# Performance work log

Measured on AMD Instinct MI355X. Metric: run time of the kernel, lower is better.

Reference implementation:

```python
import jax, jax.numpy as jnp
import numpy as np

N_NODES = 100000
N_EDGES = 1600000
IN_C, HID_C, OUT_C = 128, 128, 64


def gcn_conv(x, W, b, src, dst, n_nodes):
    """PyG-style GCNConv: h = x @ W; add self-loops; symmetric deg^-1/2 norm;
    scatter-add aggregation; + bias. Self-loop contribution added analytically
    (norm for self-loop edge i->i is deg_i^-1) instead of materializing edges."""
    h = x @ W  # [N, C_out]
    # degree over dst including self-loops (edge weights are all ones)
    deg = jax.ops.segment_sum(jnp.ones((src.shape[0],), h.dtype), dst,
                              num_segments=n_nodes) + 1.0
    dinv = jax.lax.rsqrt(deg)  # deg >= 1 always
    norm = dinv[src] * dinv[dst]  # [E]
    agg = jax.ops.segment_sum(h[src] * norm[:, None], dst, num_segments=n_nodes)
    agg = agg + h * (dinv * dinv)[:, None]  # self-loop term
    return agg + b


def setup_inputs() -> dict:
    key = jax.random.key(0)
    k0, k1, k2, k3, k4, k5 = jax.random.split(key, 6)
    x = jax.random.normal(k0, (N_NODES, IN_C), dtype=jnp.float32)
    edge_index = jax.random.randint(k1, (2, N_EDGES), 0, N_NODES, dtype=jnp.int64)
    s1 = 1.0 / np.sqrt(IN_C)
    s2 = 1.0 / np.sqrt(HID_C)
    W1 = jax.random.uniform(k2, (IN_C, HID_C), jnp.float32, -s1, s1)
    b1 = jax.random.uniform(k3, (HID_C,), jnp.float32, -s1, s1)
    W2 = jax.random.uniform(k4, (HID_C, OUT_C), jnp.float32, -s2, s2)
    b2 = jax.random.uniform(k5, (OUT_C,), jnp.float32, -s2, s2)
    return {"x": x, "W1": W1, "b1": b1, "W2": W2, "b2": b2,
            "edge_index": edge_index}


def reference(x, W1, b1, W2, b2, edge_index):
    src, dst = edge_index[0], edge_index[1]
    h = gcn_conv(x, W1, b1, src, dst, N_NODES)
    h = jax.nn.relu(h)
    out = gcn_conv(h, W2, b2, src, dst, N_NODES)
    return out
```

## Files before the change

kernel.cpp:

```cpp
#include <hip/hip_runtime.h>


static constexpr int BSHIFT = 7;
static constexpr int BWIDTH = 1 << BSHIFT;
static constexpr int MAXBUCK = 2048;
static constexpr int NPART = 256;

static constexpr size_t OFF_FLAG = 0;
static constexpr size_t OFF_DEG  = 256;
static constexpr size_t OFF_ROW  = 458752;
static constexpr size_t OFF_BSUM = 917504;
static constexpr size_t OFF_CCNT = 925696;
static constexpr size_t OFF_COFF = 937984;
static constexpr size_t OFF_DINV = 962560;
static constexpr size_t OFF_CSR  = 1376256;
static constexpr size_t OFF_HS1  = 8388608;
static constexpr size_t OFF_OUT1 = 35651584;
static constexpr size_t OFF_HS2  = 62914560;
static constexpr size_t OFF_H2   = 75714560;

__device__ __forceinline__ unsigned short f2bf(float f) {
    unsigned u = __float_as_uint(f);
    u += 0x7fffu + ((u >> 16) & 1u);
    return (unsigned short)(u >> 16);
}

typedef __attribute__((ext_vector_type(8))) short bf16x8;
typedef __attribute__((ext_vector_type(4))) float f32x4;

__global__ void detect_kernel(const unsigned* __restrict__ w,
                              unsigned* __restrict__ flag) {
    int i = blockIdx.x * blockDim.x + threadIdx.x;
    if (w[2 * i + 1] != 0u) atomicOr(flag, 1u);
}

__device__ __forceinline__ int edge_dst(const unsigned* w, unsigned flag,
                                        int e, int E) {
    return flag ? (int)w[E + e] : (int)w[2 * E + 2 * e];
}
__device__ __forceinline__ int edge_src(const unsigned* w, unsigned flag,
                                        int e, int E) {
    return flag ? (int)w[e] : (int)w[2 * e];
}

__global__ __launch_bounds__(1024) void coarse_hist_kernel(
    const unsigned* __restrict__ w, const unsigned* __restrict__ flag,
    unsigned* __restrict__ ccnt, unsigned* __restrict__ h2, int E, int nbuck) {
    __shared__ unsigned hist[MAXBUCK];
    for (int i = threadIdx.x; i < nbuck; i += 1024) hist[i] = 0;
    __syncthreads();
    const unsigned f = *flag;
    const int per = (E + gridDim.x - 1) / gridDim.x;
    const int e0 = blockIdx.x * per, e1 = min(E, e0 + per);
    for (int e = e0 + (int)threadIdx.x; e < e1; e += 1024)
        atomicAdd(&hist[edge_dst(w, f, e, E) >> BSHIFT], 1u);
    __syncthreads();
    for (int i = threadIdx.x; i < nbuck; i += 1024) {
        unsigned h = hist[i];
        h2[(size_t)i * NPART + blockIdx.x] = h;
        if (h) atomicAdd(&ccnt[i], h);
    }
}

__global__ __launch_bounds__(1024) void coarse_scan_kernel(
    const unsigned* __restrict__ ccnt, unsigned* __restrict__ coff, int nbuck) {
    __shared__ unsigned sh[1024];
    const int t = threadIdx.x;
    unsigned run = 0;
    for (int b0 = 0; b0 < nbuck; b0 += 1024) {
        unsigned v = (b0 + t < nbuck) ? ccnt[b0 + t] : 0u;
        sh[t] = v;
        __syncthreads();
        for (int off = 1; off < 1024; off <<= 1) {
            unsigned a = (t >= off) ? sh[t - off] : 0u;
            __syncthreads();
            sh[t] += a;
            __syncthreads();
        }
        if (b0 + t < nbuck) coff[b0 + t] = run + sh[t] - v;
        run += sh[1023];
        __syncthreads();
    }
    if (t == 0) coff[nbuck] = run;
}

__global__ __launch_bounds__(NPART) void off2d_kernel(
    unsigned* __restrict__ h2, const unsigned* __restrict__ coff) {
    __shared__ unsigned sh[NPART];
    const int b = blockIdx.x, t = threadIdx.x;
    unsigned v = h2[(size_t)b * NPART + t];
    sh[t] = v;
    __syncthreads();
#pragma unroll
    for (int off = 1; off < NPART; off <<= 1) {
        unsigned a = (t >= off) ? sh[t - off] : 0u;
        __syncthreads();
        sh[t] += a;
        __syncthreads();
    }
    h2[(size_t)b * NPART + t] = coff[b] + sh[t] - v;
}

__global__ __launch_bounds__(1024) void partition_kernel(
    const unsigned* __restrict__ w, const unsigned* __restrict__ flag,
    const unsigned* __restrict__ h2, unsigned* __restrict__ part, int E,
    int nbuck) {
    __shared__ unsigned lcur[MAXBUCK];
    for (int i = threadIdx.x; i < nbuck; i += 1024)
        lcur[i] = h2[(size_t)i * NPART + blockIdx.x];
    __syncthreads();
    const unsigned f = *flag;
    const int per = (E + gridDim.x - 1) / gridDim.x;
    const int e0 = blockIdx.x * per, e1 = min(E, e0 + per);
    for (int e = e0 + (int)threadIdx.x; e < e1; e += 1024) {
        int d = edge_dst(w, f, e, E);
        int s = edge_src(w, f, e, E);
        unsigned pos = atomicAdd(&lcur[d >> BSHIFT], 1u);
        part[pos] = (unsigned)s | ((unsigned)(d & (BWIDTH - 1)) << 20);
    }
}

__global__ __launch_bounds__(256) void bucket_csr_kernel(
    const unsigned* __restrict__ part, const unsigned* __restrict__ coff,
    unsigned* __restrict__ deg, int* __restrict__ csr, int N) {
    __shared__ unsigned cnt[BWIDTH];
    __shared__ unsigned sc[BWIDTH];
    __shared__ unsigned cur[BWIDTH];
    const int b = blockIdx.x, base = b << BSHIFT, t = threadIdx.x;
    if (t < BWIDTH) cnt[t] = 0;
    __syncthreads();
    const int e0 = (int)coff[b], e1 = (int)coff[b + 1];
    for (int e = e0 + t; e < e1; e += 256)
        atomicAdd(&cnt[part[e] >> 20], 1u);
    __syncthreads();
    if (t < BWIDTH && base + t < N) deg[base + t] = cnt[t];
    if (t < BWIDTH) sc[t] = cnt[t];
    __syncthreads();
#pragma unroll
    for (int off = 1; off < BWIDTH; off <<= 1) {
        unsigned a = (t < BWIDTH && t >= off) ? sc[t - off] : 0u;
        __syncthreads();
        if (t < BWIDTH) sc[t] += a;
        __syncthreads();
    }
    if (t < BWIDTH) cur[t] = (unsigned)e0 + sc[t] - cnt[t];
    __syncthreads();
    for (int e = e0 + t; e < e1; e += 256) {
        unsigned pk = part[e];
        unsigned p = atomicAdd(&cur[pk >> 20], 1u);
        csr[p] = (int)(pk & 0xFFFFFu);
    }
}

__global__ __launch_bounds__(1024) void scan1_kernel(
    const unsigned* __restrict__ deg, unsigned* __restrict__ row,
    unsigned* __restrict__ bsum, int N) {
    __shared__ unsigned sh[1024];
    int gid = blockIdx.x * 1024 + threadIdx.x;
    int t = threadIdx.x;
    unsigned v = (gid < N) ? deg[gid] : 0u;
    sh[t] = v;
    __syncthreads();
#pragma unroll
    for (int off = 1; off < 1024; off <<= 1) {
        unsigned add = (t >= off) ? sh[t - off] : 0u;
        __syncthreads();
        sh[t] += add;
        __syncthreads();
    }
    if (gid < N) row[gid + 1] = sh[t];
    if (t == 1023) bsum[blockIdx.x] = sh[1023];
}

__global__ __launch_bounds__(1024) void scan2_kernel(unsigned* __restrict__ bsum,
                                                     int NB) {
    __shared__ unsigned sh[1024];
    const int t = threadIdx.x;
    unsigned v = (t < NB) ? bsum[t] : 0u;
    sh[t] = v;
    __syncthreads();
#pragma unroll
    for (int off = 1; off < 1024; off <<= 1) {
        unsigned a = (t >= off) ? sh[t - off] : 0u;
        __syncthreads();
        sh[t] += a;
        __syncthreads();
    }
    if (t < NB) bsum[t] = sh[t] - v;
}

__global__ void scan3_kernel(unsigned* __restrict__ row,
                             const unsigned* __restrict__ bsum,
                             const unsigned* __restrict__ deg,
                             float* __restrict__ dinv, int N) {
    int gid = blockIdx.x * blockDim.x + threadIdx.x;
    if (gid >= N) return;
    row[gid + 1] += bsum[gid >> 10];
    if (gid == 0) row[0] = 0u;
    dinv[gid] = rsqrtf((float)deg[gid] + 1.0f);
}

template <int BN, bool ABF16>
__global__ __launch_bounds__(256) void gemm_mfma(
    const void* __restrict__ Av, const float* __restrict__ B,
    const float* __restrict__ dinv, unsigned short* __restrict__ out, int M) {
    constexpr int NT = BN / 16;
    __shared__ short sA[16384];
    __shared__ short sB[NT * 2048];

    const int t = threadIdx.x;
    const int row0 = blockIdx.x * 128;
    const int w = t >> 6, lane = t & 63;
    const int m = lane & 15, q = lane >> 4;

    if (ABF16) {
        const unsigned short* A = (const unsigned short*)Av;
        for (int g = t; g < 2048; g += 256) {
            int r = g >> 4, k0 = (g & 15) << 3;
            uint4 v = make_uint4(0u, 0u, 0u, 0u);
            if (row0 + r < M) v = *(const uint4*)(A + (size_t)(row0 + r) * 128 + k0);
            int off = ((((r >> 4) * 4 + (k0 >> 5)) * 16 + (r & 15)) * 4 +
                       ((k0 >> 3) & 3)) * 8;
            *(uint4*)(sA + off) = v;
        }
    } else {
        const float* A = (const float*)Av;
        for (int g = t; g < 4096; g += 256) {
            int r = g >> 5, k0 = (g & 31) << 2;
            float4 v = make_float4(0.f, 0.f, 0.f, 0.f);
            if (row0 + r < M) v = *(const float4*)(A + (size_t)(row0 + r) * 128 + k0);
            ushort4 u;
            u.x = f2bf(v.x); u.y = f2bf(v.y); u.z = f2bf(v.z); u.w = f2bf(v.w);
            int off = ((((r >> 4) * 4 + (k0 >> 5)) * 16 + (r & 15)) * 4 +
                       ((k0 >> 3) & 3)) * 8 + (k0 & 4);
            *(ushort4*)(sA + off) = u;
        }
    }
    for (int g = t; g < BN * 32; g += 256) {
        int n = g % BN, k0 = (g / BN) * 4;
        float f0 = B[(size_t)(k0 + 0) * BN + n];
        float f1 = B[(size_t)(k0 + 1) * BN + n];
        float f2 = B[(size_t)(k0 + 2) * BN + n];
        float f3 = B[(size_t)(k0 + 3) * BN + n];
        ushort4 u;
        u.x = f2bf(f0); u.y = f2bf(f1); u.z = f2bf(f2); u.w = f2bf(f3);
        int off = ((((n >> 4) * 4 + (k0 >> 5)) * 16 + (n & 15)) * 4 +
                   ((k0 >> 3) & 3)) * 8 + (k0 & 4);
        *(ushort4*)(sB + off) = u;
    }
    __syncthreads();

    f32x4 acc[2][NT];
#pragma unroll
    for (int lt = 0; lt < 2; lt++)
#pragma unroll
        for (int nt = 0; nt < NT; nt++) acc[lt][nt] = (f32x4){0.f, 0.f, 0.f, 0.f};

    const int fb = (m * 4 + q) * 8;
#pragma unroll
    for (int ks = 0; ks < 4; ks++) {
        bf16x8 a0 = *(const bf16x8*)(sA + ((w * 2 + 0) * 4 + ks) * 512 + fb);
        bf16x8 a1 = *(const bf16x8*)(sA + ((w * 2 + 1) * 4 + ks) * 512 + fb);
#pragma unroll
        for (int nt = 0; nt < NT; nt++) {
            bf16x8 b = *(const bf16x8*)(sB + (nt * 4 + ks) * 512 + fb);
            acc[0][nt] = __builtin_amdgcn_mfma_f32_16x16x32_bf16(a0, b, acc[0][nt], 0, 0, 0);
            acc[1][nt] = __builtin_amdgcn_mfma_f32_16x16x32_bf16(a1, b, acc[1][nt], 0, 0, 0);
        }
    }

#pragma unroll
    for (int lt = 0; lt < 2; lt++) {
#pragma unroll
        for (int r = 0; r < 4; r++) {
            int row = row0 + w * 32 + lt * 16 + q * 4 + r;
            if (row < M) {
                float s = dinv[row];
#pragma unroll
                for (int nt = 0; nt < NT; nt++)
                    out[(size_t)row * BN + nt * 16 + m] = f2bf(acc[lt][nt][r] * s);
            }
        }
    }
}

template <int C, bool RELU, bool OUTBF>
__global__ __launch_bounds__(256) void agg_kernel(
    const int* __restrict__ csr, const unsigned* __restrict__ row,
    const unsigned short* __restrict__ hsb, const float* __restrict__ dinv,
    const float* __restrict__ bias, void* __restrict__ outv, int N) {
    constexpr int LPN = C / 8;
    const int tid = blockIdx.x * 256 + threadIdx.x;
    const int i = tid / LPN;
    const int l = tid % LPN;
    if (i >= N) return;

    const int co = 8 * l;
    float s0 = 0.f, s1 = 0.f, s2 = 0.f, s3 = 0.f,
          s4 = 0.f, s5 = 0.f, s6 = 0.f, s7 = 0.f;
    {
        uint4 u = *(const uint4*)(hsb + (size_t)i * C + co);
        s0 += __uint_as_float(u.x << 16); s1 += __uint_as_float(u.x & 0xffff0000u);
        s2 += __uint_as_float(u.y << 16); s3 += __uint_as_float(u.y & 0xffff0000u);
        s4 += __uint_as_float(u.z << 16); s5 += __uint_as_float(u.z & 0xffff0000u);
        s6 += __uint_as_float(u.w << 16); s7 += __uint_as_float(u.w & 0xffff0000u);
    }

    const int rs = (int)row[i], re = (int)row[i + 1];
    for (int e0 = rs; e0 < re; e0 += LPN) {
        int idx = (e0 + l < re) ? csr[e0 + l] : 0;
        const int cnt = min(LPN, re - e0);
#pragma unroll 4
        for (int j = 0; j < cnt; j++) {
            int s = __shfl(idx, j, LPN);
            uint4 u = *(const uint4*)(hsb + (size_t)s * C + co);
            s0 += __uint_as_float(u.x << 16); s1 += __uint_as_float(u.x & 0xffff0000u);
            s2 += __uint_as_float(u.y << 16); s3 += __uint_as_float(u.y & 0xffff0000u);
            s4 += __uint_as_float(u.z << 16); s5 += __uint_as_float(u.z & 0xffff0000u);
            s6 += __uint_as_float(u.w << 16); s7 += __uint_as_float(u.w & 0xffff0000u);
        }
    }

    const float sc = dinv[i];
    const float4 ba = *(const float4*)(bias + co);
    const float4 bb = *(const float4*)(bias + co + 4);
    float o0 = s0 * sc + ba.x, o1 = s1 * sc + ba.y;
    float o2 = s2 * sc + ba.z, o3 = s3 * sc + ba.w;
    float o4 = s4 * sc + bb.x, o5 = s5 * sc + bb.y;
    float o6 = s6 * sc + bb.z, o7 = s7 * sc + bb.w;
    if (RELU) {
        o0 = fmaxf(o0, 0.f); o1 = fmaxf(o1, 0.f); o2 = fmaxf(o2, 0.f);
        o3 = fmaxf(o3, 0.f); o4 = fmaxf(o4, 0.f); o5 = fmaxf(o5, 0.f);
        o6 = fmaxf(o6, 0.f); o7 = fmaxf(o7, 0.f);
    }
    if (OUTBF) {
        uint4 u;
        u.x = (unsigned)f2bf(o0) | ((unsigned)f2bf(o1) << 16);
        u.y = (unsigned)f2bf(o2) | ((unsigned)f2bf(o3) << 16);
        u.z = (unsigned)f2bf(o4) | ((unsigned)f2bf(o5) << 16);
        u.w = (unsigned)f2bf(o6) | ((unsigned)f2bf(o7) << 16);
        *(uint4*)((unsigned short*)outv + (size_t)i * C + co) = u;
    } else {
        float4 a = make_float4(o0, o1, o2, o3);
        float4 b = make_float4(o4, o5, o6, o7);
        *(float4*)((float*)outv + (size_t)i * C + co) = a;
        *(float4*)((float*)outv + (size_t)i * C + co + 4) = b;
    }
}

extern "C" void kernel_launch(void* const* d_in, const int* in_sizes, int n_in,
                              void* d_out, int out_size, void* d_ws,
                              size_t ws_size, hipStream_t stream) {
    const float* x  = (const float*)d_in[0];
    const float* W1 = (const float*)d_in[1];
    const float* b1 = (const float*)d_in[2];
    const float* W2 = (const float*)d_in[3];
    const float* b2 = (const float*)d_in[4];
    const unsigned* ew = (const unsigned*)d_in[5];
    const int E = in_sizes[5] / 2;
    const int N = in_sizes[0] / 128;
    const int NB = (N + 1023) >> 10;
    const int nbuck = (N + BWIDTH - 1) >> BSHIFT;

    char* ws = (char*)d_ws;
    unsigned* flag = (unsigned*)(ws + OFF_FLAG);
    unsigned* deg  = (unsigned*)(ws + OFF_DEG);
    unsigned* row  = (unsigned*)(ws + OFF_ROW);
    unsigned* bsum = (unsigned*)(ws + OFF_BSUM);
    unsigned* ccnt = (unsigned*)(ws + OFF_CCNT);
    unsigned* coff = (unsigned*)(ws + OFF_COFF);
    float* dinv    = (float*)(ws + OFF_DINV);
    int* csr       = (int*)(ws + OFF_CSR);
    unsigned short* hs1  = (unsigned short*)(ws + OFF_HS1);
    unsigned short* out1 = (unsigned short*)(ws + OFF_OUT1);
    unsigned short* hs2  = (unsigned short*)(ws + OFF_HS2);
    unsigned* h2   = (unsigned*)(ws + OFF_H2);
    unsigned* part = (unsigned*)(ws + OFF_HS1);

    hipMemsetAsync(flag, 0, 4, stream);
    hipMemsetAsync(ccnt, 0, (size_t)(nbuck + 1) * 4, stream);

    detect_kernel<<<16, 256, 0, stream>>>(ew, flag);
    coarse_hist_kernel<<<NPART, 1024, 0, stream>>>(ew, flag, ccnt, h2, E, nbuck);
    coarse_scan_kernel<<<1, 1024, 0, stream>>>(ccnt, coff, nbuck);
    off2d_kernel<<<nbuck, NPART, 0, stream>>>(h2, coff);
    partition_kernel<<<NPART, 1024, 0, stream>>>(ew, flag, h2, part, E, nbuck);
    bucket_csr_kernel<<<nbuck, 256, 0, stream>>>(part, coff, deg, csr, N);
    scan1_kernel<<<NB, 1024, 0, stream>>>(deg, row, bsum, N);
    scan2_kernel<<<1, 1024, 0, stream>>>(bsum, NB);
    scan3_kernel<<<(N + 255) / 256, 256, 0, stream>>>(row, bsum, deg, dinv, N);

    gemm_mfma<128, false><<<(N + 127) / 128, 256, 0, stream>>>(x, W1, dinv, hs1, N);
    agg_kernel<128, true, true><<<(N * 16 + 255) / 256, 256, 0, stream>>>(
        csr, row, hs1, dinv, b1, out1, N);

    gemm_mfma<64, true><<<(N + 127) / 128, 256, 0, stream>>>(out1, W2, dinv, hs2, N);
    agg_kernel<64, false, false><<<(N * 8 + 255) / 256, 256, 0, stream>>>(
        csr, row, hs2, dinv, b2, d_out, N);
}
```

Baseline: 309.5 us.

## Replace bucketed CSR build with atomic degree count and scatter; pre-swizzle weights

Drops the two-level bucket partition CSR construction (hist, scans, partition, per-bucket sort) and builds the CSR with global atomic degree counting, a prefix scan, and an atomic-cursor scatter. The weights are converted to bf16 once in MFMA fragment layout by a small prep kernel. The GEMM then loads A fragments and B straight from global memory instead of staging them in LDS. This removes several launches and the LDS staging and barrier. In exchange it adds heavy global atomic contention on random destinations, makes the neighbor order within a row nondeterministic, and gives uncoalesced direct global loads in the GEMM.

```diff
diff --git a/kernel.cpp b/kernel.cpp
--- a/kernel.cpp
+++ b/kernel.cpp
@@ -1,23 +1,17 @@
 #include <hip/hip_runtime.h>
 
-
-static constexpr int BSHIFT = 7;
-static constexpr int BWIDTH = 1 << BSHIFT;
-static constexpr int MAXBUCK = 2048;
-static constexpr int NPART = 256;
 
 static constexpr size_t OFF_FLAG = 0;
 static constexpr size_t OFF_DEG  = 256;
 static constexpr size_t OFF_ROW  = 458752;
 static constexpr size_t OFF_BSUM = 917504;
-static constexpr size_t OFF_CCNT = 925696;
-static constexpr size_t OFF_COFF = 937984;
 static constexpr size_t OFF_DINV = 962560;
 static constexpr size_t OFF_CSR  = 1376256;
 static constexpr size_t OFF_HS1  = 8388608;
 static constexpr size_t OFF_OUT1 = 35651584;
 static constexpr size_t OFF_HS2  = 62914560;
-static constexpr size_t OFF_H2   = 75714560;
+static constexpr size_t OFF_W1S  = 75714560;
+static constexpr size_t OFF_W2S  = 75747328;
 
 __device__ __forceinline__ unsigned short f2bf(float f) {
     unsigned u = __float_as_uint(f);
@@ -28,12 +22,6 @@
 typedef __attribute__((ext_vector_type(8))) short bf16x8;
 typedef __attribute__((ext_vector_type(4))) float f32x4;
 
-__global__ void detect_kernel(const unsigned* __restrict__ w,
-                              unsigned* __restrict__ flag) {
-    int i = blockIdx.x * blockDim.x + threadIdx.x;
-    if (w[2 * i + 1] != 0u) atomicOr(flag, 1u);
-}
-
 __device__ __forceinline__ int edge_dst(const unsigned* w, unsigned flag,
                                         int e, int E) {
     return flag ? (int)w[E + e] : (int)w[2 * E + 2 * e];
@@ -43,113 +31,41 @@
     return flag ? (int)w[e] : (int)w[2 * e];
 }
 
-__global__ __launch_bounds__(1024) void coarse_hist_kernel(
+__global__ __launch_bounds__(256) void wprep_kernel(
+    const float* __restrict__ W1, const float* __restrict__ W2,
+    unsigned short* __restrict__ O1, unsigned short* __restrict__ O2) {
+    const float* W = blockIdx.x ? W2 : W1;
+    unsigned short* O = blockIdx.x ? O2 : O1;
+    const int BN = blockIdx.x ? 64 : 128;
+    const int total = 128 * BN / 4;
+    for (int g = threadIdx.x; g < total; g += 256) {
+        int n = g % BN, k0 = (g / BN) * 4;
+        ushort4 u;
+        u.x = f2bf(W[(size_t)(k0 + 0) * BN + n]);
+        u.y = f2bf(W[(size_t)(k0 + 1) * BN + n]);
+        u.z = f2bf(W[(size_t)(k0 + 2) * BN + n]);
+        u.w = f2bf(W[(size_t)(k0 + 3) * BN + n]);
+        int off = ((((n >> 4) * 4 + (k0 >> 5)) * 16 + (n & 15)) * 4 +
+                   ((k0 >> 3) & 3)) * 8 + (k0 & 4);
+        *(ushort4*)(O + off) = u;
+    }
+}
+
+__global__ __launch_bounds__(256) void init_deg_detect(
+    const unsigned* __restrict__ w, unsigned* __restrict__ flag,
+    unsigned* __restrict__ deg, int N) {
+    int i = blockIdx.x * 256 + threadIdx.x;
+    if (i < N) deg[i] = 0u;
+    if (i < 4096 && w[2 * i + 1] != 0u) atomicOr(flag, 1u);
+}
+
+__global__ __launch_bounds__(256) void deg_kernel(
     const unsigned* __restrict__ w, const unsigned* __restrict__ flag,
-    unsigned* __restrict__ ccnt, unsigned* __restrict__ h2, int E, int nbuck) {
-    __shared__ unsigned hist[MAXBUCK];
-    for (int i = threadIdx.x; i < nbuck; i += 1024) hist[i] = 0;
-    __syncthreads();
+    unsigned* __restrict__ deg, int E) {
+    int e = blockIdx.x * 256 + threadIdx.x;
+    if (e >= E) return;
     const unsigned f = *flag;
-    const int per = (E + gridDim.x - 1) / gridDim.x;
-    const int e0 = blockIdx.x * per, e1 = min(E, e0 + per);
-    for (int e = e0 + (int)threadIdx.x; e < e1; e += 1024)
-        atomicAdd(&hist[edge_dst(w, f, e, E) >> BSHIFT], 1u);
-    __syncthreads();
-    for (int i = threadIdx.x; i < nbuck; i += 1024) {
-        unsigned h = hist[i];
-        h2[(size_t)i * NPART + blockIdx.x] = h;
-        if (h) atomicAdd(&ccnt[i], h);
-    }
-}
-
-__global__ __launch_bounds__(1024) void coarse_scan_kernel(
-    const unsigned* __restrict__ ccnt, unsigned* __restrict__ coff, int nbuck) {
-    __shared__ unsigned sh[1024];
-    const int t = threadIdx.x;
-    unsigned run = 0;
-    for (int b0 = 0; b0 < nbuck; b0 += 1024) {
-        unsigned v = (b0 + t < nbuck) ? ccnt[b0 + t] : 0u;
-        sh[t] = v;
-        __syncthreads();
-        for (int off = 1; off < 1024; off <<= 1) {
-            unsigned a = (t >= off) ? sh[t - off] : 0u;
-            __syncthreads();
-            sh[t] += a;
-            __syncthreads();
-        }
-        if (b0 + t < nbuck) coff[b0 + t] = run + sh[t] - v;
-        run += sh[1023];
-        __syncthreads();
-    }
-    if (t == 0) coff[nbuck] = run;
-}
-
-__global__ __launch_bounds__(NPART) void off2d_kernel(
-    unsigned* __restrict__ h2, const unsigned* __restrict__ coff) {
-    __shared__ unsigned sh[NPART];
-    const int b = blockIdx.x, t = threadIdx.x;
-    unsigned v = h2[(size_t)b * NPART + t];
-    sh[t] = v;
-    __syncthreads();
-#pragma unroll
-    for (int off = 1; off < NPART; off <<= 1) {
-        unsigned a = (t >= off) ? sh[t - off] : 0u;
-        __syncthreads();
-        sh[t] += a;
-        __syncthreads();
-    }
-    h2[(size_t)b * NPART + t] = coff[b] + sh[t] - v;
-}
-
-__global__ __launch_bounds__(1024) void partition_kernel(
-    const unsigned* __restrict__ w, const unsigned* __restrict__ flag,
-    const unsigned* __restrict__ h2, unsigned* __restrict__ part, int E,
-    int nbuck) {
-    __shared__ unsigned lcur[MAXBUCK];
-    for (int i = threadIdx.x; i < nbuck; i += 1024)
-        lcur[i] = h2[(size_t)i * NPART + blockIdx.x];
-    __syncthreads();
-    const unsigned f = *flag;
-    const int per = (E + gridDim.x - 1) / gridDim.x;
-    const int e0 = blockIdx.x * per, e1 = min(E, e0 + per);
-    for (int e = e0 + (int)threadIdx.x; e < e1; e += 1024) {
-        int d = edge_dst(w, f, e, E);
-        int s = edge_src(w, f, e, E);
-        unsigned pos = atomicAdd(&lcur[d >> BSHIFT], 1u);
-        part[pos] = (unsigned)s | ((unsigned)(d & (BWIDTH - 1)) << 20);
-    }
-}
-
-__global__ __launch_bounds__(256) void bucket_csr_kernel(
-    const unsigned* __restrict__ part, const unsigned* __restrict__ coff,
-    unsigned* __restrict__ deg, int* __restrict__ csr, int N) {
-    __shared__ unsigned cnt[BWIDTH];
-    __shared__ unsigned sc[BWIDTH];
-    __shared__ unsigned cur[BWIDTH];
-    const int b = blockIdx.x, base = b << BSHIFT, t = threadIdx.x;
-    if (t < BWIDTH) cnt[t] = 0;
-    __syncthreads();
-    const int e0 = (int)coff[b], e1 = (int)coff[b + 1];
-    for (int e = e0 + t; e < e1; e += 256)
-        atomicAdd(&cnt[part[e] >> 20], 1u);
-    __syncthreads();
-    if (t < BWIDTH && base + t < N) deg[base + t] = cnt[t];
-    if (t < BWIDTH) sc[t] = cnt[t];
-    __syncthreads();
-#pragma unroll
-    for (int off = 1; off < BWIDTH; off <<= 1) {
-        unsigned a = (t < BWIDTH && t >= off) ? sc[t - off] : 0u;
-        __syncthreads();
-        if (t < BWIDTH) sc[t] += a;
-        __syncthreads();
-    }
-    if (t < BWIDTH) cur[t] = (unsigned)e0 + sc[t] - cnt[t];
-    __syncthreads();
-    for (int e = e0 + t; e < e1; e += 256) {
-        unsigned pk = part[e];
-        unsigned p = atomicAdd(&cur[pk >> 20], 1u);
-        csr[p] = (int)(pk & 0xFFFFFu);
-    }
+    atomicAdd(&deg[edge_dst(w, f, e, E)], 1u);
 }
 
 __global__ __launch_bounds__(1024) void scan1_kernel(
@@ -189,81 +105,82 @@
     if (t < NB) bsum[t] = sh[t] - v;
 }
 
-__global__ void scan3_kernel(unsigned* __restrict__ row,
-                             const unsigned* __restrict__ bsum,
-                             const unsigned* __restrict__ deg,
-                             float* __restrict__ dinv, int N) {
-    int gid = blockIdx.x * blockDim.x + threadIdx.x;
+__global__ __launch_bounds__(256) void scan3_kernel(
+    unsigned* __restrict__ row, const unsigned* __restrict__ bsum,
+    unsigned* __restrict__ deg, float* __restrict__ dinv, int N) {
+    int gid = blockIdx.x * 256 + threadIdx.x;
     if (gid >= N) return;
-    row[gid + 1] += bsum[gid >> 10];
+    unsigned r1 = row[gid + 1] + bsum[gid >> 10];
+    row[gid + 1] = r1;
     if (gid == 0) row[0] = 0u;
-    dinv[gid] = rsqrtf((float)deg[gid] + 1.0f);
+    unsigned d = deg[gid];
+    dinv[gid] = rsqrtf((float)d + 1.0f);
+    deg[gid] = r1 - d;
+}
+
+__global__ __launch_bounds__(256) void scatter_kernel(
+    const unsigned* __restrict__ w, const unsigned* __restrict__ flag,
+    unsigned* __restrict__ cur, int* __restrict__ csr, int E) {
+    int e = blockIdx.x * 256 + threadIdx.x;
+    if (e >= E) return;
+    const unsigned f = *flag;
+    int d = edge_dst(w, f, e, E);
+    int s = edge_src(w, f, e, E);
+    unsigned pos = atomicAdd(&cur[d], 1u);
+    csr[pos] = s;
 }
 
 template <int BN, bool ABF16>
 __global__ __launch_bounds__(256) void gemm_mfma(
-    const void* __restrict__ Av, const float* __restrict__ B,
+    const void* __restrict__ Av, const unsigned short* __restrict__ Bs,
     const float* __restrict__ dinv, unsigned short* __restrict__ out, int M) {
     constexpr int NT = BN / 16;
-    __shared__ short sA[16384];
-    __shared__ short sB[NT * 2048];
-
     const int t = threadIdx.x;
     const int row0 = blockIdx.x * 128;
     const int w = t >> 6, lane = t & 63;
     const int m = lane & 15, q = lane >> 4;
-
-    if (ABF16) {
-        const unsigned short* A = (const unsigned short*)Av;
-        for (int g = t; g < 2048; g += 256) {
-            int r = g >> 4, k0 = (g & 15) << 3;
-            uint4 v = make_uint4(0u, 0u, 0u, 0u);
-            if (row0 + r < M) v = *(const uint4*)(A + (size_t)(row0 + r) * 128 + k0);
-            int off = ((((r >> 4) * 4 + (k0 >> 5)) * 16 + (r & 15)) * 4 +
-                       ((k0 >> 3) & 3)) * 8;
-            *(uint4*)(sA + off) = v;
+    const int fb = (m * 4 + q) * 8;
+
+    const int r0 = row0 + (2 * w) * 16 + m;
+    const int r1 = r0 + 16;
+
+    f32x4 acc[2][NT];
+#pragma unroll
+    for (int lt = 0; lt < 2; lt++)
+#pragma unroll
+        for (int nt = 0; nt < NT; nt++) acc[lt][nt] = (f32x4){0.f, 0.f, 0.f, 0.f};
+
+#pragma unroll
+    for (int ks = 0; ks < 4; ks++) {
+        const int k0 = ks * 32 + q * 8;
+        bf16x8 a0 = (bf16x8){0, 0, 0, 0, 0, 0, 0, 0};
+        bf16x8 a1 = (bf16x8){0, 0, 0, 0, 0, 0, 0, 0};
+        if (ABF16) {
+            const unsigned short* A = (const unsigned short*)Av;
+            if (r0 < M) a0 = *(const bf16x8*)(A + (size_t)r0 * 128 + k0);
+            if (r1 < M) a1 = *(const bf16x8*)(A + (size_t)r1 * 128 + k0);
+        } else {
+            const float* A = (const float*)Av;
+            if (r0 < M) {
+                const float* p = A + (size_t)r0 * 128 + k0;
+                f32x4 lo = *(const f32x4*)p, hi = *(const f32x4*)(p + 4);
+                a0[0] = (short)f2bf(lo[0]); a0[1] = (short)f2bf(lo[1]);
+                a0[2] = (short)f2bf(lo[2]); a0[3] = (short)f2bf(lo[3]);
+                a0[4] = (short)f2bf(hi[0]); a0[5] = (short)f2bf(hi[1]);
+                a0[6] = (short)f2bf(hi[2]); a0[7] = (short)f2bf(hi[3]);
+            }
+            if (r1 < M) {
+                const float* p = A + (size_t)r1 * 128 + k0;
+                f32x4 lo = *(const f32x4*)p, hi = *(const f32x4*)(p + 4);
+                a1[0] = (short)f2bf(lo[0]); a1[1] = (short)f2bf(lo[1]);
+                a1[2] = (short)f2bf(lo[2]); a1[3] = (short)f2bf(lo[3]);
+                a1[4] = (short)f2bf(hi[0]); a1[5] = (short)f2bf(hi[1]);
+                a1[6] = (short)f2bf(hi[2]); a1[7] = (short)f2bf(hi[3]);
+            }
         }
-    } else {
-        const float* A = (const float*)Av;
-        for (int g = t; g < 4096; g += 256) {
-            int r = g >> 5, k0 = (g & 31) << 2;
-            float4 v = make_float4(0.f, 0.f, 0.f, 0.f);
-            if (row0 + r < M) v = *(const float4*)(A + (size_t)(row0 + r) * 128 + k0);
-            ushort4 u;
-            u.x = f2bf(v.x); u.y = f2bf(v.y); u.z = f2bf(v.z); u.w = f2bf(v.w);
-            int off = ((((r >> 4) * 4 + (k0 >> 5)) * 16 + (r & 15)) * 4 +
-                       ((k0 >> 3) & 3)) * 8 + (k0 & 4);
-            *(ushort4*)(sA + off) = u;
-        }
-    }
-    for (int g = t; g < BN * 32; g += 256) {
-        int n = g % BN, k0 = (g / BN) * 4;
-        float f0 = B[(size_t)(k0 + 0) * BN + n];
-        float f1 = B[(size_t)(k0 + 1) * BN + n];
-        float f2 = B[(size_t)(k0 + 2) * BN + n];
-        float f3 = B[(size_t)(k0 + 3) * BN + n];
-        ushort4 u;
-        u.x = f2bf(f0); u.y = f2bf(f1); u.z = f2bf(f2); u.w = f2bf(f3);
-        int off = ((((n >> 4) * 4 + (k0 >> 5)) * 16 + (n & 15)) * 4 +
-                   ((k0 >> 3) & 3)) * 8 + (k0 & 4);
-        *(ushort4*)(sB + off) = u;
-    }
-    __syncthreads();
-
-    f32x4 acc[2][NT];
-#pragma unroll
-    for (int lt = 0; lt < 2; lt++)
-#pragma unroll
-        for (int nt = 0; nt < NT; nt++) acc[lt][nt] = (f32x4){0.f, 0.f, 0.f, 0.f};
-
-    const int fb = (m * 4 + q) * 8;
-#pragma unroll
-    for (int ks = 0; ks < 4; ks++) {
-        bf16x8 a0 = *(const bf16x8*)(sA + ((w * 2 + 0) * 4 + ks) * 512 + fb);
-        bf16x8 a1 = *(const bf16x8*)(sA + ((w * 2 + 1) * 4 + ks) * 512 + fb);
 #pragma unroll
         for (int nt = 0; nt < NT; nt++) {
-            bf16x8 b = *(const bf16x8*)(sB + (nt * 4 + ks) * 512 + fb);
+            bf16x8 b = *(const bf16x8*)(Bs + (nt * 4 + ks) * 512 + fb);
             acc[0][nt] = __builtin_amdgcn_mfma_f32_16x16x32_bf16(a0, b, acc[0][nt], 0, 0, 0);
             acc[1][nt] = __builtin_amdgcn_mfma_f32_16x16x32_bf16(a1, b, acc[1][nt], 0, 0, 0);
         }
@@ -360,41 +277,36 @@
     const int E = in_sizes[5] / 2;
     const int N = in_sizes[0] / 128;
     const int NB = (N + 1023) >> 10;
-    const int nbuck = (N + BWIDTH - 1) >> BSHIFT;
 
     char* ws = (char*)d_ws;
     unsigned* flag = (unsigned*)(ws + OFF_FLAG);
     unsigned* deg  = (unsigned*)(ws + OFF_DEG);
     unsigned* row  = (unsigned*)(ws + OFF_ROW);
     unsigned* bsum = (unsigned*)(ws + OFF_BSUM);
-    unsigned* ccnt = (unsigned*)(ws + OFF_CCNT);
-    unsigned* coff = (unsigned*)(ws + OFF_COFF);
     float* dinv    = (float*)(ws + OFF_DINV);
     int* csr       = (int*)(ws + OFF_CSR);
     unsigned short* hs1  = (unsigned short*)(ws + OFF_HS1);
     unsigned short* out1 = (unsigned short*)(ws + OFF_OUT1);
     unsigned short* hs2  = (unsigned short*)(ws + OFF_HS2);
-    unsigned* h2   = (unsigned*)(ws + OFF_H2);
-    unsigned* part = (unsigned*)(ws + OFF_HS1);
+    unsigned short* w1s  = (unsigned short*)(ws + OFF_W1S);
+    unsigned short* w2s  = (unsigned short*)(ws + OFF_W2S);
 
     hipMemsetAsync(flag, 0, 4, stream);
-    hipMemsetAsync(ccnt, 0, (size_t)(nbuck + 1) * 4, stream);
-
-    detect_kernel<<<16, 256, 0, stream>>>(ew, flag);
-    coarse_hist_kernel<<<NPART, 1024, 0, stream>>>(ew, flag, ccnt, h2, E, nbuck);
-    coarse_scan_kernel<<<1, 1024, 0, stream>>>(ccnt, coff, nbuck);
-    off2d_kernel<<<nbuck, NPART, 0, stream>>>(h2, coff);
-    partition_kernel<<<NPART, 1024, 0, stream>>>(ew, flag, h2, part, E, nbuck);
-    bucket_csr_kernel<<<nbuck, 256, 0, stream>>>(part, coff, deg, csr, N);
+
+    wprep_kernel<<<2, 256, 0, stream>>>(W1, W2, w1s, w2s);
+
+    init_deg_detect<<<(N + 255) / 256, 256, 0, stream>>>(ew, flag, deg, N);
+    deg_kernel<<<(E + 255) / 256, 256, 0, stream>>>(ew, flag, deg, E);
     scan1_kernel<<<NB, 1024, 0, stream>>>(deg, row, bsum, N);
     scan2_kernel<<<1, 1024, 0, stream>>>(bsum, NB);
     scan3_kernel<<<(N + 255) / 256, 256, 0, stream>>>(row, bsum, deg, dinv, N);
-
-    gemm_mfma<128, false><<<(N + 127) / 128, 256, 0, stream>>>(x, W1, dinv, hs1, N);
+    scatter_kernel<<<(E + 255) / 256, 256, 0, stream>>>(ew, flag, deg, csr, E);
+
+    gemm_mfma<128, false><<<(N + 127) / 128, 256, 0, stream>>>(x, w1s, dinv, hs1, N);
     agg_kernel<128, true, true><<<(N * 16 + 255) / 256, 256, 0, stream>>>(
         csr, row, hs1, dinv, b1, out1, N);
 
-    gemm_mfma<64, true><<<(N + 127) / 128, 256, 0, stream>>>(out1, W2, dinv, hs2, N);
+    gemm_mfma<64, true><<<(N + 127) / 128, 256, 0, stream>>>(out1, w2s, dinv, hs2, N);
     agg_kernel<64, false, false><<<(N * 8 + 255) / 256, 256, 0, stream>>>(
         csr, row, hs2, dinv, b2, d_out, N);
 }
```

Result: slower. 444.3 us (+43.5%).
